# Performance work log

Measured on AMD Instinct MI355X. Metric: run time of the kernel, lower is better.

The kernel has to match this reference:

```python
import jax, jax.numpy as jnp
import numpy as np

B, SQ, SK, D = 8, 4096, 4096, 64


def setup_inputs() -> dict:
    key = jax.random.key(0)
    k1, k2, k3 = jax.random.split(key, 3)
    x1 = jax.random.normal(k1, (B, SQ, D), dtype=jnp.float32)   # queries
    x2 = jax.random.normal(k2, (B, SK, D), dtype=jnp.float32)   # keys
    x3 = jax.random.normal(k3, (B, SK, D), dtype=jnp.float32)   # values
    x4 = 0                                                      # dropout p (static, 0 => deterministic)
    x5 = jnp.ones((1,), dtype=jnp.float32)                      # scale divisor
    return {"x1": x1, "x2": x2, "x3": x3, "x4": x4, "x5": x5}


def reference(x1, x2, x3, x4, x5):
    # scores: [B, Sq, Sk]
    scores = jnp.einsum("bqd,bkd->bqk", x1, x2) / x5
    attn = jax.nn.softmax(scores, axis=-1)
    p = float(x4)  # static python scalar
    if p > 0.0:
        mask = jax.random.bernoulli(jax.random.key(42), 1.0 - p, attn.shape)
        attn = attn * mask.astype(attn.dtype) / (1.0 - p)
    # out: [B, Sq, D]
    return jnp.einsum("bqk,bkd->bqd", attn, x3)
```

## Files before the change

kernel.cpp:

```cpp
#include <hip/hip_runtime.h>


typedef _Float16 f16x8 __attribute__((ext_vector_type(8)));
typedef _Float16 f16x4 __attribute__((ext_vector_type(4)));
typedef __fp16   h16x2 __attribute__((ext_vector_type(2)));
typedef float    f32x4 __attribute__((ext_vector_type(4)));
typedef float    f32x16 __attribute__((ext_vector_type(16)));

constexpr int kB  = 8;
constexpr int kSQ = 4096;
constexpr int kSK = 4096;
constexpr int kD  = 64;
constexpr int KSPLIT = 4;
constexpr int SKH = kSK / KSPLIT;
constexpr int BQ  = 256;
constexpr int MT  = 2;
constexpr int BK  = 64;
constexpr int TK  = 128;
constexpr size_t APART = (size_t)kB * kSQ * kD;
constexpr float kLog2e = 1.44269504088896340736f;
constexpr float kDeferThr = 11.5f;

static __device__ __forceinline__ f16x4 pack4(float a, float b, float c, float d) {
    h16x2 p0 = __builtin_amdgcn_cvt_pkrtz(a, b);
    h16x2 p1 = __builtin_amdgcn_cvt_pkrtz(c, d);
    f16x4 r;
    r[0] = (_Float16)p0[0]; r[1] = (_Float16)p0[1];
    r[2] = (_Float16)p1[0]; r[3] = (_Float16)p1[1];
    return r;
}
static __device__ __forceinline__ f16x8 pack8(const float4& a, const float4& c) {
    f16x4 lo = pack4(a.x, a.y, a.z, a.w);
    f16x4 hi = pack4(c.x, c.y, c.z, c.w);
    f16x8 f;
    f[0] = lo[0]; f[1] = lo[1]; f[2] = lo[2]; f[3] = lo[3];
    f[4] = hi[0]; f[5] = hi[1]; f[6] = hi[2]; f[7] = hi[3];
    return f;
}
static __device__ __forceinline__ unsigned pkrtz_u(float a, float b) {
    union { h16x2 h; unsigned u; } cv;
    cv.h = __builtin_amdgcn_cvt_pkrtz(a, b);
    return cv.u;
}
static __device__ __forceinline__ float xhalf_max(float x) {
    union { float f; unsigned u; } uv; uv.f = x;
    auto pr = __builtin_amdgcn_permlane32_swap(uv.u, uv.u, false, false);
    union { unsigned u; float f; } r0, r1;
    r0.u = pr[0]; r1.u = pr[1];
    return fmaxf(r0.f, r1.f);
}

typedef const __attribute__((address_space(1))) unsigned int* gu32p;
typedef __attribute__((address_space(3))) unsigned int* lu32p;
static __device__ __forceinline__ void gload_lds16(const void* g, void* l) {
    __builtin_amdgcn_global_load_lds((gu32p)g, (lu32p)l, 16, 0, 0);
}

#define PA_SLICE(dst, sv, rb) do {                                          \
    unsigned c0 = pkrtz_u((sv)[(rb)+0], (sv)[(rb)+1]);                      \
    unsigned c1 = pkrtz_u((sv)[(rb)+2], (sv)[(rb)+3]);                      \
    unsigned c2 = pkrtz_u((sv)[(rb)+4], (sv)[(rb)+5]);                      \
    unsigned c3 = pkrtz_u((sv)[(rb)+6], (sv)[(rb)+7]);                      \
    auto r02 = __builtin_amdgcn_permlane32_swap(c0, c2, false, false);      \
    auto r13 = __builtin_amdgcn_permlane32_swap(c1, c3, false, false);      \
    union { unsigned u[4]; f16x8 v; } _r;                                   \
    _r.u[0] = r02[0]; _r.u[1] = r13[0]; _r.u[2] = r02[1]; _r.u[3] = r13[1]; \
    dst = _r.v;                                                             \
} while (0)

__global__ __launch_bounds__(256, 2)
void fattn_prepass(const float* __restrict__ Kg,
                   const float* __restrict__ Vg,
                   _Float16* __restrict__ Kh,
                   _Float16* __restrict__ Vt)
{
    __shared__ _Float16 tr[kD][BK];

    const int tid = threadIdx.x;
    const int kt  = blockIdx.x;
    const int b   = blockIdx.y;

    const int k = tid >> 2;
    const int p = tid & 3;
    const int gk = kt * BK + k;

    {
        const float* src = Kg + ((size_t)b * kSK + gk) * kD + p * 16;
        const float4 a0 = *(const float4*)(src + 0);
        const float4 a1 = *(const float4*)(src + 4);
        const float4 a2 = *(const float4*)(src + 8);
        const float4 a3 = *(const float4*)(src + 12);
        _Float16* dst = Kh + ((size_t)b * kSK + gk) * kD;
        const int fb0 = 2 * p, fb1 = 2 * p + 1;
        *(f16x8*)&dst[(fb0 ^ (gk & 7)) * 8] = pack8(a0, a1);
        *(f16x8*)&dst[(fb1 ^ (gk & 7)) * 8] = pack8(a2, a3);
    }
    {
        const float* src = Vg + ((size_t)b * kSK + gk) * kD + p * 16;
        const float4 a0 = *(const float4*)(src + 0);
        const float4 a1 = *(const float4*)(src + 4);
        const float4 a2 = *(const float4*)(src + 8);
        const float4 a3 = *(const float4*)(src + 12);
        const float v[16] = {a0.x,a0.y,a0.z,a0.w, a1.x,a1.y,a1.z,a1.w,
                             a2.x,a2.y,a2.z,a2.w, a3.x,a3.y,a3.z,a3.w};
#pragma unroll
        for (int j = 0; j < 16; ++j)
            tr[p * 16 + j][k] = (_Float16)v[j];
    }
    __syncthreads();
    {
        const int f  = tid >> 2;
        const int p2 = tid & 3;
        const f16x8 b0 = *(const f16x8*)&tr[f][p2 * 16 + 0];
        const f16x8 b1 = *(const f16x8*)&tr[f][p2 * 16 + 8];
        _Float16* dst = Vt + (((size_t)b * 64 + kt) * kD + f) * BK;
        const int kb0 = 2 * p2, kb1 = 2 * p2 + 1;
        *(f16x8*)&dst[(kb0 ^ (f & 7)) * 8] = b0;
        *(f16x8*)&dst[(kb1 ^ (f & 7)) * 8] = b1;
    }
}

__global__ __launch_bounds__(256, 2)
void fattn_partial(const float* __restrict__ Qg,
                   const _Float16* __restrict__ Kh,
                   const _Float16* __restrict__ Vt,
                   const float* __restrict__ sdiv,
                   _Float16* __restrict__ Ap,
                   float2* __restrict__ MLp)
{
    __shared__ __align__(16) _Float16 sK[2][TK * kD];
    __shared__ __align__(16) _Float16 sV[2][kD * TK];

    const int tid  = threadIdx.x;
    const int w    = tid >> 6;
    const int lane = tid & 63;
    const int l31  = lane & 31;
    const int hi   = lane >> 5;

    const int flat = blockIdx.x;
    const int c    = flat & 31;
    const int qi   = flat >> 5;
    const int b    = c >> 2;
    const int ks   = c & 3;
    const int qb   = qi * BQ;

    const float qscale = kLog2e / sdiv[0];

    const float* Qb = Qg + ((size_t)b * kSQ + qb) * kD;
    const _Float16* Khb = Kh + ((size_t)b * kSK + (size_t)ks * SKH) * kD;
    const _Float16* Vtb = Vt + (((size_t)b * 64 + (size_t)ks * (SKH / BK)) * kD) * BK;

    f16x8 qf[MT][4];
#pragma unroll
    for (int mt = 0; mt < MT; ++mt) {
        const float* qrow = Qb + (size_t)(w * 64 + mt * 32 + l31) * kD;
#pragma unroll
        for (int ds = 0; ds < 4; ++ds) {
            const float4 a  = *(const float4*)(qrow + ds * 16 + hi * 8);
            const float4 cc = *(const float4*)(qrow + ds * 16 + hi * 8 + 4);
            float4 as = make_float4(a.x * qscale, a.y * qscale, a.z * qscale, a.w * qscale);
            float4 cs = make_float4(cc.x * qscale, cc.y * qscale, cc.z * qscale, cc.w * qscale);
            qf[mt][ds] = pack8(as, cs);
        }
    }

    f16x8 ones;
#pragma unroll
    for (int j = 0; j < 8; ++j) ones[j] = (_Float16)1.0f;

    int offA[4];
#pragma unroll
    for (int i = 0; i < 4; ++i)
        offA[i] = l31 * 64 + (((2 * i + hi) ^ (l31 & 7)) * 8);

    auto stage = [&](int kt, int buf) {
        const char* gk = (const char*)(Khb + (size_t)kt * TK * kD) + w * 4096 + lane * 16;
        const char* gv = (const char*)(Vtb + (size_t)kt * kD * TK) + w * 4096 + lane * 16;
        char* lk = (char*)&sK[buf][0] + w * 4096;
        char* lv = (char*)&sV[buf][0] + w * 4096;
        gload_lds16(gk,        lk);
        gload_lds16(gk + 1024, lk + 1024);
        gload_lds16(gk + 2048, lk + 2048);
        gload_lds16(gk + 3072, lk + 3072);
        gload_lds16(gv,        lv);
        gload_lds16(gv + 1024, lv + 1024);
        gload_lds16(gv + 2048, lv + 2048);
        gload_lds16(gv + 3072, lv + 3072);
    };

    f32x16 oL[MT], oH[MT];
    f32x16 ol[MT];
    float m_i[MT];
#pragma unroll
    for (int mt = 0; mt < MT; ++mt) {
        m_i[mt] = -1e30f;
#pragma unroll
        for (int r = 0; r < 16; ++r) { oL[mt][r] = 0.0f; oH[mt][r] = 0.0f; ol[mt][r] = 0.0f; }
    }

    stage(0, 0);
    __syncthreads();

    const int nIter = SKH / TK;
    for (int kt = 0; kt < nIter; ++kt) {
        const int buf = kt & 1;
        if (kt + 1 < nIter) stage(kt + 1, buf ^ 1);

#pragma unroll
        for (int sub = 0; sub < 2; ++sub) {
            const int sb = sub * (BK * kD);

            f16x8 kf0[4], kf1[4];
#pragma unroll
            for (int ds = 0; ds < 4; ++ds) {
                kf0[ds] = *(const f16x8*)&sK[buf][sb + offA[ds]];
                kf1[ds] = *(const f16x8*)&sK[buf][sb + offA[ds] + 2048];
            }

            f32x16 s0[MT], s1[MT];
#pragma unroll
            for (int mt = 0; mt < MT; ++mt)
#pragma unroll
                for (int r = 0; r < 16; ++r) { s0[mt][r] = 0.0f; s1[mt][r] = 0.0f; }

            __builtin_amdgcn_s_setprio(1);
#pragma unroll
            for (int ds = 0; ds < 4; ++ds)
#pragma unroll
                for (int mt = 0; mt < MT; ++mt) {
                    s0[mt] = __builtin_amdgcn_mfma_f32_32x32x16_f16(kf0[ds], qf[mt][ds], s0[mt], 0, 0, 0);
                    s1[mt] = __builtin_amdgcn_mfma_f32_32x32x16_f16(kf1[ds], qf[mt][ds], s1[mt], 0, 0, 0);
                }
            __builtin_amdgcn_s_setprio(0);

            f16x8 vf[4][2];
#pragma unroll
            for (int s = 0; s < 4; ++s) {
                vf[s][0] = *(const f16x8*)&sV[buf][sb + offA[s]];
                vf[s][1] = *(const f16x8*)&sV[buf][sb + offA[s] + 2048];
            }

#pragma unroll
            for (int mt = 0; mt < MT; ++mt) {
                float t[16];
#pragma unroll
                for (int r = 0; r < 16; ++r) t[r] = fmaxf(s0[mt][r], s1[mt][r]);
#pragma unroll
                for (int r = 0; r < 8; ++r)  t[r] = fmaxf(t[r], t[r + 8]);
#pragma unroll
                for (int r = 0; r < 4; ++r)  t[r] = fmaxf(t[r], t[r + 4]);
                float rm = fmaxf(fmaxf(t[0], t[1]), fmaxf(t[2], t[3]));
                rm = xhalf_max(rm);

                if (!__all(rm <= m_i[mt] + kDeferThr)) {
                    const float mnew  = fmaxf(m_i[mt], rm);
                    const float alpha = __builtin_amdgcn_exp2f(m_i[mt] - mnew);
                    ol[mt][0] *= alpha;
#pragma unroll
                    for (int r = 0; r < 16; ++r) { oL[mt][r] *= alpha; oH[mt][r] *= alpha; }
                    m_i[mt] = mnew;
                }

#pragma unroll
                for (int r = 0; r < 16; ++r) {
                    s0[mt][r] = __builtin_amdgcn_exp2f(s0[mt][r] - m_i[mt]);
                    s1[mt][r] = __builtin_amdgcn_exp2f(s1[mt][r] - m_i[mt]);
                }

                f16x8 pa[4];
                PA_SLICE(pa[0], s0[mt], 0);
                PA_SLICE(pa[1], s0[mt], 8);
                PA_SLICE(pa[2], s1[mt], 0);
                PA_SLICE(pa[3], s1[mt], 8);

                __builtin_amdgcn_s_setprio(1);
#pragma unroll
                for (int s = 0; s < 4; ++s) {
                    oL[mt] = __builtin_amdgcn_mfma_f32_32x32x16_f16(vf[s][0], pa[s], oL[mt], 0, 0, 0);
                    oH[mt] = __builtin_amdgcn_mfma_f32_32x32x16_f16(vf[s][1], pa[s], oH[mt], 0, 0, 0);
                    ol[mt] = __builtin_amdgcn_mfma_f32_32x32x16_f16(ones,     pa[s], ol[mt], 0, 0, 0);
                }
                __builtin_amdgcn_s_setprio(0);
            }
        }

        __syncthreads();
    }

    _Float16* Ab = Ap + (size_t)ks * APART + ((size_t)b * kSQ + qb) * kD;
    float2* MLb = MLp + (size_t)ks * kB * kSQ + (size_t)b * kSQ + qb;
#pragma unroll
    for (int mt = 0; mt < MT; ++mt) {
        const int q = w * 64 + mt * 32 + l31;
        const float lf = ol[mt][0];
        const float inv = 1.0f / lf;
        _Float16* arow = &Ab[(size_t)q * kD];
#pragma unroll
        for (int g = 0; g < 4; ++g) {
            *(f16x4*)&arow[g * 8 + hi * 4] =
                pack4(oL[mt][4 * g] * inv, oL[mt][4 * g + 1] * inv,
                      oL[mt][4 * g + 2] * inv, oL[mt][4 * g + 3] * inv);
            *(f16x4*)&arow[32 + g * 8 + hi * 4] =
                pack4(oH[mt][4 * g] * inv, oH[mt][4 * g + 1] * inv,
                      oH[mt][4 * g + 2] * inv, oH[mt][4 * g + 3] * inv);
        }
        if (hi == 0) MLb[q] = make_float2(m_i[mt], lf);
    }
}

__global__ __launch_bounds__(256)
void fattn_combine(const _Float16* __restrict__ Ap,
                   const float2* __restrict__ MLp,
                   float* __restrict__ Og)
{
    const int idx = blockIdx.x * 256 + threadIdx.x;
    const int r = idx >> 4;
    const int c = (idx & 15) * 4;

    float m = -1e30f;
    float2 ml[KSPLIT];
#pragma unroll
    for (int s = 0; s < KSPLIT; ++s) {
        ml[s] = MLp[(size_t)s * kB * kSQ + r];
        m = fmaxf(m, ml[s].x);
    }
    float acc[4] = {0.f, 0.f, 0.f, 0.f};
    float lsum = 0.f;
#pragma unroll
    for (int s = 0; s < KSPLIT; ++s) {
        const float wgt = __builtin_amdgcn_exp2f(ml[s].x - m) * ml[s].y;
        lsum += wgt;
        const f16x4 a = *(const f16x4*)&Ap[(size_t)s * APART + (size_t)r * kD + c];
#pragma unroll
        for (int j = 0; j < 4; ++j) acc[j] += wgt * (float)a[j];
    }
    const float inv = 1.0f / lsum;
    float4 res = make_float4(acc[0] * inv, acc[1] * inv, acc[2] * inv, acc[3] * inv);
    *(float4*)&Og[(size_t)r * kD + c] = res;
}

extern "C" void kernel_launch(void* const* d_in, const int* in_sizes, int n_in,
                              void* d_out, int out_size, void* d_ws, size_t ws_size,
                              hipStream_t stream) {
    const float* Q    = (const float*)d_in[0];
    const float* K    = (const float*)d_in[1];
    const float* V    = (const float*)d_in[2];
    const float* sdiv = (const float*)d_in[4];
    float* O = (float*)d_out;

    _Float16* Kh  = (_Float16*)d_ws;
    _Float16* Vt  = Kh + (size_t)kB * kSK * kD;
    _Float16* Ap  = Vt + (size_t)kB * kSK * kD;
    float2*   MLp = (float2*)(Ap + (size_t)KSPLIT * APART);

    fattn_prepass<<<dim3(kSK / BK, kB), dim3(256), 0, stream>>>(K, V, Kh, Vt);
    fattn_partial<<<dim3((kSQ / BQ) * kB * KSPLIT), dim3(256), 0, stream>>>(Q, Kh, Vt, sdiv, Ap, MLp);
    fattn_combine<<<dim3(kB * kSQ * kD / (256 * 4)), dim3(256), 0, stream>>>(Ap, MLp, O);
}
```

Before: 135.0 us.

## Fuse split-K partial attention and combine into one workgroup via LDS

The partial and combine kernels are merged into one kernel. Each 512-thread block handles 128 queries, and its 8 waves are split into 4 key-range groups by 2 query halves. Per-split partial outputs and (m, l) statistics go to shared memory instead of global, and the block merges them before writing the final output. This removes the global round trip for partials and one kernel launch. In exchange, each wave processes 64-key tiles with its own double buffer, the block uses 128 KB of LDS, and the grid shrinks to 256 blocks, which may limit occupancy.

```diff
diff --git a/kernel.cpp b/kernel.cpp
--- a/kernel.cpp
+++ b/kernel.cpp
@@ -13,11 +13,10 @@
 constexpr int kD  = 64;
 constexpr int KSPLIT = 4;
 constexpr int SKH = kSK / KSPLIT;
-constexpr int BQ  = 256;
+constexpr int BQ  = 128;
 constexpr int MT  = 2;
 constexpr int BK  = 64;
-constexpr int TK  = 128;
-constexpr size_t APART = (size_t)kB * kSQ * kD;
+constexpr int PSTR = 72;
 constexpr float kLog2e = 1.44269504088896340736f;
 constexpr float kDeferThr = 11.5f;
 
@@ -120,28 +119,30 @@
     }
 }
 
-__global__ __launch_bounds__(256, 2)
-void fattn_partial(const float* __restrict__ Qg,
-                   const _Float16* __restrict__ Kh,
-                   const _Float16* __restrict__ Vt,
-                   const float* __restrict__ sdiv,
-                   _Float16* __restrict__ Ap,
-                   float2* __restrict__ MLp)
+__global__ __launch_bounds__(512, 2)
+void fattn_fused(const float* __restrict__ Qg,
+                 const _Float16* __restrict__ Kh,
+                 const _Float16* __restrict__ Vt,
+                 const float* __restrict__ sdiv,
+                 float* __restrict__ Og)
 {
-    __shared__ __align__(16) _Float16 sK[2][TK * kD];
-    __shared__ __align__(16) _Float16 sV[2][kD * TK];
+    __shared__ __align__(16) char smem[131072];
+    _Float16* sKb = (_Float16*)smem;
+    _Float16* sVb = (_Float16*)(smem + 65536);
+    _Float16* sPart = (_Float16*)smem;
+    float2*   sMl   = (float2*)(smem + (size_t)2 * 4 * 64 * PSTR * 2);
 
     const int tid  = threadIdx.x;
     const int w    = tid >> 6;
     const int lane = tid & 63;
     const int l31  = lane & 31;
     const int hi   = lane >> 5;
+    const int ks   = w & 3;
+    const int mh   = w >> 2;
 
     const int flat = blockIdx.x;
-    const int c    = flat & 31;
-    const int qi   = flat >> 5;
-    const int b    = c >> 2;
-    const int ks   = c & 3;
+    const int b    = flat & 7;
+    const int qi   = flat >> 3;
     const int qb   = qi * BQ;
 
     const float qscale = kLog2e / sdiv[0];
@@ -150,10 +151,13 @@
     const _Float16* Khb = Kh + ((size_t)b * kSK + (size_t)ks * SKH) * kD;
     const _Float16* Vtb = Vt + (((size_t)b * 64 + (size_t)ks * (SKH / BK)) * kD) * BK;
 
+    _Float16* sK = sKb + (ks * 2) * 4096;
+    _Float16* sV = sVb + (ks * 2) * 4096;
+
     f16x8 qf[MT][4];
 #pragma unroll
     for (int mt = 0; mt < MT; ++mt) {
-        const float* qrow = Qb + (size_t)(w * 64 + mt * 32 + l31) * kD;
+        const float* qrow = Qb + (size_t)(mh * 64 + mt * 32 + l31) * kD;
 #pragma unroll
         for (int ds = 0; ds < 4; ++ds) {
             const float4 a  = *(const float4*)(qrow + ds * 16 + hi * 8);
@@ -174,10 +178,10 @@
         offA[i] = l31 * 64 + (((2 * i + hi) ^ (l31 & 7)) * 8);
 
     auto stage = [&](int kt, int buf) {
-        const char* gk = (const char*)(Khb + (size_t)kt * TK * kD) + w * 4096 + lane * 16;
-        const char* gv = (const char*)(Vtb + (size_t)kt * kD * TK) + w * 4096 + lane * 16;
-        char* lk = (char*)&sK[buf][0] + w * 4096;
-        char* lv = (char*)&sV[buf][0] + w * 4096;
+        const char* gk = (const char*)(Khb + (size_t)kt * BK * kD) + mh * 4096 + lane * 16;
+        const char* gv = (const char*)(Vtb + (size_t)kt * kD * BK) + mh * 4096 + lane * 16;
+        char* lk = (char*)&sK[buf * 4096] + mh * 4096;
+        char* lv = (char*)&sV[buf * 4096] + mh * 4096;
         gload_lds16(gk,        lk);
         gload_lds16(gk + 1024, lk + 1024);
         gload_lds16(gk + 2048, lk + 2048);
@@ -201,142 +205,143 @@
     stage(0, 0);
     __syncthreads();
 
-    const int nIter = SKH / TK;
+    const int nIter = SKH / BK;
     for (int kt = 0; kt < nIter; ++kt) {
         const int buf = kt & 1;
         if (kt + 1 < nIter) stage(kt + 1, buf ^ 1);
 
-#pragma unroll
-        for (int sub = 0; sub < 2; ++sub) {
-            const int sb = sub * (BK * kD);
-
-            f16x8 kf0[4], kf1[4];
-#pragma unroll
-            for (int ds = 0; ds < 4; ++ds) {
-                kf0[ds] = *(const f16x8*)&sK[buf][sb + offA[ds]];
-                kf1[ds] = *(const f16x8*)&sK[buf][sb + offA[ds] + 2048];
-            }
-
-            f32x16 s0[MT], s1[MT];
-#pragma unroll
-            for (int mt = 0; mt < MT; ++mt)
-#pragma unroll
-                for (int r = 0; r < 16; ++r) { s0[mt][r] = 0.0f; s1[mt][r] = 0.0f; }
+        f16x8 kf0[4], kf1[4];
+#pragma unroll
+        for (int ds = 0; ds < 4; ++ds) {
+            kf0[ds] = *(const f16x8*)&sK[buf * 4096 + offA[ds]];
+            kf1[ds] = *(const f16x8*)&sK[buf * 4096 + offA[ds] + 2048];
+        }
+
+        f32x16 s0[MT], s1[MT];
+#pragma unroll
+        for (int mt = 0; mt < MT; ++mt)
+#pragma unroll
+            for (int r = 0; r < 16; ++r) { s0[mt][r] = 0.0f; s1[mt][r] = 0.0f; }
+
+        __builtin_amdgcn_s_setprio(1);
+#pragma unroll
+        for (int ds = 0; ds < 4; ++ds)
+#pragma unroll
+            for (int mt = 0; mt < MT; ++mt) {
+                s0[mt] = __builtin_amdgcn_mfma_f32_32x32x16_f16(kf0[ds], qf[mt][ds], s0[mt], 0, 0, 0);
+                s1[mt] = __builtin_amdgcn_mfma_f32_32x32x16_f16(kf1[ds], qf[mt][ds], s1[mt], 0, 0, 0);
+            }
+        __builtin_amdgcn_s_setprio(0);
+
+        f16x8 vf[4][2];
+#pragma unroll
+        for (int s = 0; s < 4; ++s) {
+            vf[s][0] = *(const f16x8*)&sV[buf * 4096 + offA[s]];
+            vf[s][1] = *(const f16x8*)&sV[buf * 4096 + offA[s] + 2048];
+        }
+
+#pragma unroll
+        for (int mt = 0; mt < MT; ++mt) {
+            float t[16];
+#pragma unroll
+            for (int r = 0; r < 16; ++r) t[r] = fmaxf(s0[mt][r], s1[mt][r]);
+#pragma unroll
+            for (int r = 0; r < 8; ++r)  t[r] = fmaxf(t[r], t[r + 8]);
+#pragma unroll
+            for (int r = 0; r < 4; ++r)  t[r] = fmaxf(t[r], t[r + 4]);
+            float rm = fmaxf(fmaxf(t[0], t[1]), fmaxf(t[2], t[3]));
+            rm = xhalf_max(rm);
+
+            if (!__all(rm <= m_i[mt] + kDeferThr)) {
+                const float mnew  = fmaxf(m_i[mt], rm);
+                const float alpha = __builtin_amdgcn_exp2f(m_i[mt] - mnew);
+                ol[mt][0] *= alpha;
+#pragma unroll
+                for (int r = 0; r < 16; ++r) { oL[mt][r] *= alpha; oH[mt][r] *= alpha; }
+                m_i[mt] = mnew;
+            }
+
+#pragma unroll
+            for (int r = 0; r < 16; ++r) {
+                s0[mt][r] = __builtin_amdgcn_exp2f(s0[mt][r] - m_i[mt]);
+                s1[mt][r] = __builtin_amdgcn_exp2f(s1[mt][r] - m_i[mt]);
+            }
+
+            f16x8 pa[4];
+            PA_SLICE(pa[0], s0[mt], 0);
+            PA_SLICE(pa[1], s0[mt], 8);
+            PA_SLICE(pa[2], s1[mt], 0);
+            PA_SLICE(pa[3], s1[mt], 8);
 
             __builtin_amdgcn_s_setprio(1);
 #pragma unroll
-            for (int ds = 0; ds < 4; ++ds)
-#pragma unroll
-                for (int mt = 0; mt < MT; ++mt) {
-                    s0[mt] = __builtin_amdgcn_mfma_f32_32x32x16_f16(kf0[ds], qf[mt][ds], s0[mt], 0, 0, 0);
-                    s1[mt] = __builtin_amdgcn_mfma_f32_32x32x16_f16(kf1[ds], qf[mt][ds], s1[mt], 0, 0, 0);
-                }
+            for (int s = 0; s < 4; ++s) {
+                oL[mt] = __builtin_amdgcn_mfma_f32_32x32x16_f16(vf[s][0], pa[s], oL[mt], 0, 0, 0);
+                oH[mt] = __builtin_amdgcn_mfma_f32_32x32x16_f16(vf[s][1], pa[s], oH[mt], 0, 0, 0);
+                ol[mt] = __builtin_amdgcn_mfma_f32_32x32x16_f16(ones,     pa[s], ol[mt], 0, 0, 0);
+            }
             __builtin_amdgcn_s_setprio(0);
-
-            f16x8 vf[4][2];
-#pragma unroll
-            for (int s = 0; s < 4; ++s) {
-                vf[s][0] = *(const f16x8*)&sV[buf][sb + offA[s]];
-                vf[s][1] = *(const f16x8*)&sV[buf][sb + offA[s] + 2048];
-            }
-
-#pragma unroll
-            for (int mt = 0; mt < MT; ++mt) {
-                float t[16];
-#pragma unroll
-                for (int r = 0; r < 16; ++r) t[r] = fmaxf(s0[mt][r], s1[mt][r]);
-#pragma unroll
-                for (int r = 0; r < 8; ++r)  t[r] = fmaxf(t[r], t[r + 8]);
-#pragma unroll
-                for (int r = 0; r < 4; ++r)  t[r] = fmaxf(t[r], t[r + 4]);
-                float rm = fmaxf(fmaxf(t[0], t[1]), fmaxf(t[2], t[3]));
-                rm = xhalf_max(rm);
-
-                if (!__all(rm <= m_i[mt] + kDeferThr)) {
-                    const float mnew  = fmaxf(m_i[mt], rm);
-                    const float alpha = __builtin_amdgcn_exp2f(m_i[mt] - mnew);
-                    ol[mt][0] *= alpha;
-#pragma unroll
-                    for (int r = 0; r < 16; ++r) { oL[mt][r] *= alpha; oH[mt][r] *= alpha; }
-                    m_i[mt] = mnew;
-                }
-
-#pragma unroll
-                for (int r = 0; r < 16; ++r) {
-                    s0[mt][r] = __builtin_amdgcn_exp2f(s0[mt][r] - m_i[mt]);
-                    s1[mt][r] = __builtin_amdgcn_exp2f(s1[mt][r] - m_i[mt]);
-                }
-
-                f16x8 pa[4];
-                PA_SLICE(pa[0], s0[mt], 0);
-                PA_SLICE(pa[1], s0[mt], 8);
-                PA_SLICE(pa[2], s1[mt], 0);
-                PA_SLICE(pa[3], s1[mt], 8);
-
-                __builtin_amdgcn_s_setprio(1);
-#pragma unroll
-                for (int s = 0; s < 4; ++s) {
-                    oL[mt] = __builtin_amdgcn_mfma_f32_32x32x16_f16(vf[s][0], pa[s], oL[mt], 0, 0, 0);
-                    oH[mt] = __builtin_amdgcn_mfma_f32_32x32x16_f16(vf[s][1], pa[s], oH[mt], 0, 0, 0);
-                    ol[mt] = __builtin_amdgcn_mfma_f32_32x32x16_f16(ones,     pa[s], ol[mt], 0, 0, 0);
-                }
-                __builtin_amdgcn_s_setprio(0);
-            }
         }
 
         __syncthreads();
     }
 
-    _Float16* Ab = Ap + (size_t)ks * APART + ((size_t)b * kSQ + qb) * kD;
-    float2* MLb = MLp + (size_t)ks * kB * kSQ + (size_t)b * kSQ + qb;
 #pragma unroll
     for (int mt = 0; mt < MT; ++mt) {
-        const int q = w * 64 + mt * 32 + l31;
+        const int ql = mt * 32 + l31;
         const float lf = ol[mt][0];
         const float inv = 1.0f / lf;
-        _Float16* arow = &Ab[(size_t)q * kD];
+        _Float16* prow = sPart + ((size_t)(mh * 4 + ks) * 64 + ql) * PSTR;
 #pragma unroll
         for (int g = 0; g < 4; ++g) {
-            *(f16x4*)&arow[g * 8 + hi * 4] =
+            *(f16x4*)&prow[g * 8 + hi * 4] =
                 pack4(oL[mt][4 * g] * inv, oL[mt][4 * g + 1] * inv,
                       oL[mt][4 * g + 2] * inv, oL[mt][4 * g + 3] * inv);
-            *(f16x4*)&arow[32 + g * 8 + hi * 4] =
+            *(f16x4*)&prow[32 + g * 8 + hi * 4] =
                 pack4(oH[mt][4 * g] * inv, oH[mt][4 * g + 1] * inv,
                       oH[mt][4 * g + 2] * inv, oH[mt][4 * g + 3] * inv);
         }
-        if (hi == 0) MLb[q] = make_float2(m_i[mt], lf);
-    }
-}
-
-__global__ __launch_bounds__(256)
-void fattn_combine(const _Float16* __restrict__ Ap,
-                   const float2* __restrict__ MLp,
-                   float* __restrict__ Og)
-{
-    const int idx = blockIdx.x * 256 + threadIdx.x;
-    const int r = idx >> 4;
-    const int c = (idx & 15) * 4;
-
-    float m = -1e30f;
-    float2 ml[KSPLIT];
-#pragma unroll
-    for (int s = 0; s < KSPLIT; ++s) {
-        ml[s] = MLp[(size_t)s * kB * kSQ + r];
-        m = fmaxf(m, ml[s].x);
-    }
-    float acc[4] = {0.f, 0.f, 0.f, 0.f};
-    float lsum = 0.f;
-#pragma unroll
-    for (int s = 0; s < KSPLIT; ++s) {
-        const float wgt = __builtin_amdgcn_exp2f(ml[s].x - m) * ml[s].y;
-        lsum += wgt;
-        const f16x4 a = *(const f16x4*)&Ap[(size_t)s * APART + (size_t)r * kD + c];
-#pragma unroll
-        for (int j = 0; j < 4; ++j) acc[j] += wgt * (float)a[j];
-    }
-    const float inv = 1.0f / lsum;
-    float4 res = make_float4(acc[0] * inv, acc[1] * inv, acc[2] * inv, acc[3] * inv);
-    *(float4*)&Og[(size_t)r * kD + c] = res;
+        if (hi == 0) sMl[(mh * 4 + ks) * 64 + ql] = make_float2(m_i[mt], lf);
+    }
+    __syncthreads();
+
+    {
+        const int qrow = tid >> 2;
+        const int cc   = (tid & 3) * 16;
+        const int emh  = qrow >> 6;
+        const int eql  = qrow & 63;
+
+        float2 ml[KSPLIT];
+        float m = -1e30f;
+#pragma unroll
+        for (int s = 0; s < KSPLIT; ++s) {
+            ml[s] = sMl[(emh * 4 + s) * 64 + eql];
+            m = fmaxf(m, ml[s].x);
+        }
+        float wgt[KSPLIT];
+        float lsum = 0.f;
+#pragma unroll
+        for (int s = 0; s < KSPLIT; ++s) {
+            wgt[s] = __builtin_amdgcn_exp2f(ml[s].x - m) * ml[s].y;
+            lsum += wgt[s];
+        }
+        const float inv = 1.0f / lsum;
+
+        float* orow = Og + (((size_t)b * kSQ + qb + qrow)) * kD + cc;
+#pragma unroll
+        for (int j = 0; j < 4; ++j) {
+            float a0 = 0.f, a1 = 0.f, a2 = 0.f, a3 = 0.f;
+#pragma unroll
+            for (int s = 0; s < KSPLIT; ++s) {
+                const f16x4 a = *(const f16x4*)&sPart[((size_t)(emh * 4 + s) * 64 + eql) * PSTR + cc + j * 4];
+                a0 += wgt[s] * (float)a[0];
+                a1 += wgt[s] * (float)a[1];
+                a2 += wgt[s] * (float)a[2];
+                a3 += wgt[s] * (float)a[3];
+            }
+            *(float4*)&orow[j * 4] = make_float4(a0 * inv, a1 * inv, a2 * inv, a3 * inv);
+        }
+    }
 }
 
 extern "C" void kernel_launch(void* const* d_in, const int* in_sizes, int n_in,
@@ -350,10 +355,7 @@
 
     _Float16* Kh  = (_Float16*)d_ws;
     _Float16* Vt  = Kh + (size_t)kB * kSK * kD;
-    _Float16* Ap  = Vt + (size_t)kB * kSK * kD;
-    float2*   MLp = (float2*)(Ap + (size_t)KSPLIT * APART);
 
     fattn_prepass<<<dim3(kSK / BK, kB), dim3(256), 0, stream>>>(K, V, Kh, Vt);
-    fattn_partial<<<dim3((kSQ / BQ) * kB * KSPLIT), dim3(256), 0, stream>>>(Q, Kh, Vt, sdiv, Ap, MLp);
-    fattn_combine<<<dim3(kB * kSQ * kD / (256 * 4)), dim3(256), 0, stream>>>(Ap, MLp, O);
-}
+    fattn_fused<<<dim3(kB * (kSQ / BQ)), dim3(512), 0, stream>>>(Q, Kh, Vt, sdiv, O);
+}
```

New measurement: 130.9 us. 1.03x faster.
